# Kernel optimization log

Measured on AMD Instinct MI355X. Metric: run time of the kernel, lower is better.

The kernel has to match this reference:

```python
import jax, jax.numpy as jnp
import numpy as np

INPUT_DIM = 512
MIX = 32
HID = 96
B, T = 256, 512


def setup_inputs() -> dict:
    key = jax.random.key(0)
    ks = jax.random.split(key, 8)
    s = lambda fan_in: 1.0 / np.sqrt(fan_in)
    x = jax.random.normal(ks[0], (B, T, INPUT_DIM), dtype=jnp.float32)
    # mix: Linear(INPUT_DIM, MIX, bias=False) -> weight [MIX, INPUT_DIM]
    W_mix = jax.random.uniform(ks[1], (MIX, INPUT_DIM), jnp.float32, -s(INPUT_DIM), s(INPUT_DIM))
    # GRU layer 0 weights, PyTorch layout: [3H, in], [3H, H], biases [3H]
    W_ih = jax.random.uniform(ks[2], (3 * HID, MIX), jnp.float32, -s(HID), s(HID))
    W_hh = jax.random.uniform(ks[3], (3 * HID, HID), jnp.float32, -s(HID), s(HID))
    b_ih = jax.random.uniform(ks[4], (3 * HID,), jnp.float32, -s(HID), s(HID))
    b_hh = jax.random.uniform(ks[5], (3 * HID,), jnp.float32, -s(HID), s(HID))
    # head: Linear(HID, MIX)
    W_head = jax.random.uniform(ks[6], (MIX, HID), jnp.float32, -s(HID), s(HID))
    b_head = jax.random.uniform(ks[7], (MIX,), jnp.float32, -s(HID), s(HID))
    return {"x": x, "W_mix": W_mix, "W_ih": W_ih, "W_hh": W_hh,
            "b_ih": b_ih, "b_hh": b_hh, "W_head": W_head, "b_head": b_head}


def _gru_last(z, W_ih, W_hh, b_ih, b_hh):
    # z: [B, T, MIX]. Precompute all input-side gate pre-activations: [T, B, 3H]
    gx = jnp.einsum('btm,gm->tbg', z, W_ih) + b_ih
    h0 = jnp.zeros((z.shape[0], HID), dtype=z.dtype)

    def step(h, gx_t):
        gh = h @ W_hh.T + b_hh  # [B, 3H]
        xr, xz, xn = jnp.split(gx_t, 3, axis=-1)
        hr, hz, hn = jnp.split(gh, 3, axis=-1)
        r = jax.nn.sigmoid(xr + hr)
        u = jax.nn.sigmoid(xz + hz)
        n = jnp.tanh(xn + r * hn)
        h_new = (1.0 - u) * n + u * h
        return h_new, None

    h_last, _ = jax.lax.scan(step, h0, gx)
    return h_last  # [B, HID]


def reference(x, W_mix, W_ih, W_hh, b_ih, b_hh, W_head, b_head):
    z = x @ W_mix.T                       # [B, T, MIX]
    last = _gru_last(z, W_ih, W_hh, b_ih, b_hh)  # [B, HID]
    z_next = last @ W_head.T + b_head     # [B, MIX]
    y_next = z_next @ W_mix               # [B, INPUT_DIM] (tied weights)
    return y_next
```

## Files before the change

kernel.cpp:

```cpp
#include <hip/hip_runtime.h>

#define IDIM 512
#define MIXD 32
#define HID 96
#define BB 256
#define TT 512
#define TROWS 32
#define SROW 516

typedef float f32x2 __attribute__((ext_vector_type(2)));
typedef float f32x4 __attribute__((ext_vector_type(4)));

#define EXP2(x) __builtin_amdgcn_exp2f(x)

template <int CTRL>
__device__ __forceinline__ float dpp_shl_add(float x) {
    int m = __builtin_amdgcn_update_dpp(0, __float_as_int(x), CTRL, 0xf, 0xf, true);
    return x + __int_as_float(m);
}
__device__ __forceinline__ float octet_reduce_lane0(float x) {
    x = dpp_shl_add<0x104>(x);
    x = dpp_shl_add<0x102>(x);
    x = dpp_shl_add<0x101>(x);
    return x;
}
__device__ __forceinline__ float red16(float x) {
    x = dpp_shl_add<0x108>(x);
    x = dpp_shl_add<0x104>(x);
    x = dpp_shl_add<0x102>(x);
    x = dpp_shl_add<0x101>(x);
    return x;
}

__global__ __launch_bounds__(256) void k_mix(const float* __restrict__ x,
                                             const float* __restrict__ Wmix,
                                             float* __restrict__ z) {
    __shared__ __align__(16) float sx[TROWS * SROW];
    const int tid = threadIdx.x;
    const int mg = tid >> 4, ks = tid & 15;

    f32x2 w0[16], w1[16];
    #pragma unroll
    for (int i = 0; i < 8; ++i) {
        const int cj = (i + ks) & 7;
        f32x4 v0 = *(const f32x4*)(Wmix + (size_t)(2 * mg)     * IDIM + ks * 32 + cj * 4);
        f32x4 v1 = *(const f32x4*)(Wmix + (size_t)(2 * mg + 1) * IDIM + ks * 32 + cj * 4);
        w0[2*i] = v0.xy; w0[2*i+1] = v0.zw;
        w1[2*i] = v1.xy; w1[2*i+1] = v1.zw;
    }

    const size_t rowbase = (size_t)blockIdx.x * 256;
    const float* xb = x + rowbase * IDIM;

    f32x4 st[16];
    #pragma unroll
    for (int i = 0; i < 16; ++i)
        st[i] = *(const f32x4*)(xb + (size_t)(tid + 256 * i) * 4);

    for (int t = 0; t < 8; ++t) {
        #pragma unroll
        for (int i = 0; i < 16; ++i) {
            const int v = tid + 256 * i, r = v >> 7, c = v & 127;
            *(f32x4*)(&sx[r * SROW + c * 4]) = st[i];
        }
        __syncthreads();

        if (t + 1 < 8) {
            const float* xn = xb + (size_t)(t + 1) * TROWS * IDIM;
            #pragma unroll
            for (int i = 0; i < 16; ++i)
                st[i] = *(const f32x4*)(xn + (size_t)(tid + 256 * i) * 4);
        }

        float* zp = z + (rowbase + (size_t)t * TROWS) * MIXD + 2 * mg;
        for (int r = 0; r < TROWS; ++r) {
            const float* rp = sx + r * SROW + ks * 32;
            f32x2 a0 = {0.f, 0.f}, a1 = {0.f, 0.f};
            #pragma unroll
            for (int i = 0; i < 8; ++i) {
                f32x4 v = *(const f32x4*)(rp + ((i + ks) & 7) * 4);
                a0 = __builtin_elementwise_fma(w0[2*i],   v.xy, a0);
                a0 = __builtin_elementwise_fma(w0[2*i+1], v.zw, a0);
                a1 = __builtin_elementwise_fma(w1[2*i],   v.xy, a1);
                a1 = __builtin_elementwise_fma(w1[2*i+1], v.zw, a1);
            }
            float s0 = red16(a0.x + a0.y);
            float s1 = red16(a1.x + a1.y);
            if (ks == 0) {
                f32x2 o2 = { s0, s1 };
                *(f32x2*)(zp + (size_t)r * MIXD) = o2;
            }
        }
        __syncthreads();
    }
}

__global__ __launch_bounds__(256, 1) void k_scan(const float* __restrict__ z,
                                                 const float* __restrict__ Wih,
                                                 const float* __restrict__ Whh,
                                                 const float* __restrict__ bih,
                                                 const float* __restrict__ bhh,
                                                 const float* __restrict__ Whead,
                                                 const float* __restrict__ bhead,
                                                 const float* __restrict__ Wmix,
                                                 float* __restrict__ y) {
    const int b   = blockIdx.x;
    const int tid = threadIdx.x;
    const int j0  = tid >> 3;
    const int o   = tid & 7;
    const float L  = 1.4426950408889634f;
    const float L2 = 2.8853900817779268f;

    __shared__ __align__(16) float sz[256 * MIXD];
    __shared__ __align__(16) float shp[2][HID];
    __shared__ __align__(16) float szn[MIXD];

    f32x2 whr[3][6], whu[3][6], whn[3][6], wir[3][2], wiu[3][2], win[3][2];
    float br[3], bu[3], bxn[3], bhn[3];
    #pragma unroll
    for (int i = 0; i < 3; ++i) {
        const int j = j0 + 32 * i;
        #pragma unroll
        for (int c = 0; c < 3; ++c) {
            f32x4 v = *(const f32x4*)(Whh + (size_t)(j        ) * HID + o * 12 + c * 4);
            v *= L;  whr[i][2*c] = v.xy; whr[i][2*c+1] = v.zw;
        }
        #pragma unroll
        for (int c = 0; c < 3; ++c) {
            f32x4 v = *(const f32x4*)(Whh + (size_t)(j +   HID) * HID + o * 12 + c * 4);
            v *= L;  whu[i][2*c] = v.xy; whu[i][2*c+1] = v.zw;
        }
        #pragma unroll
        for (int c = 0; c < 3; ++c) {
            f32x4 v = *(const f32x4*)(Whh + (size_t)(j + 2*HID) * HID + o * 12 + c * 4);
            v *= L2; whn[i][2*c] = v.xy; whn[i][2*c+1] = v.zw;
        }
        {
            f32x4 v = *(const f32x4*)(Wih + (size_t)(j        ) * MIXD + o * 4);
            v *= L;  wir[i][0] = v.xy; wir[i][1] = v.zw;
        }
        {
            f32x4 v = *(const f32x4*)(Wih + (size_t)(j +   HID) * MIXD + o * 4);
            v *= L;  wiu[i][0] = v.xy; wiu[i][1] = v.zw;
        }
        {
            f32x4 v = *(const f32x4*)(Wih + (size_t)(j + 2*HID) * MIXD + o * 4);
            v *= L2; win[i][0] = v.xy; win[i][1] = v.zw;
        }
        br[i]  = (o == 0) ? L  * (bih[j]       + bhh[j])       : 0.f;
        bu[i]  = (o == 0) ? L  * (bih[j + HID] + bhh[j + HID]) : 0.f;
        bxn[i] = (o == 0) ? L2 * bih[j + 2*HID] : 0.f;
        bhn[i] = (o == 0) ? L2 * bhh[j + 2*HID] : 0.f;
    }

    float hown[3] = {0.f, 0.f, 0.f};
    if (tid < HID) shp[0][tid] = 0.f;

    const f32x4* zb4 = (const f32x4*)(z + (size_t)b * TT * MIXD);
    f32x4* sz4 = (f32x4*)sz;

    for (int c = 0; c < TT / 256; ++c) {
        #pragma unroll
        for (int i = 0; i < 8; ++i)
            sz4[tid + 256 * i] = zb4[c * 2048 + tid + 256 * i];
        __syncthreads();

        f32x4 z4 = *(const f32x4*)(sz + 0 * MIXD + o * 4);
        for (int tt = 0; tt < 256; ++tt) {
            const int t = (c << 8) + tt;
            const float* hr = shp[t & 1];
            float*       hw = shp[(t + 1) & 1];

            const f32x4 h0 = *(const f32x4*)(hr + o * 12);
            const f32x4 h1 = *(const f32x4*)(hr + o * 12 + 4);
            const f32x4 h2 = *(const f32x4*)(hr + o * 12 + 8);
            const f32x2 hh[6] = { h0.xy, h0.zw, h1.xy, h1.zw, h2.xy, h2.zw };

            float hv[3];
            #pragma unroll
            for (int i = 0; i < 3; ++i) {
                f32x2 aR  = {br[i],  0.f}, aR2  = {0.f, 0.f};
                f32x2 aU  = {bu[i],  0.f}, aU2  = {0.f, 0.f};
                f32x2 aXN = {bxn[i], 0.f};
                f32x2 aHN = {bhn[i], 0.f}, aHN2 = {0.f, 0.f};

                aR  = __builtin_elementwise_fma(wir[i][0], z4.xy, aR);
                aR2 = __builtin_elementwise_fma(wir[i][1], z4.zw, aR2);
                aU  = __builtin_elementwise_fma(wiu[i][0], z4.xy, aU);
                aU2 = __builtin_elementwise_fma(wiu[i][1], z4.zw, aU2);
                aXN = __builtin_elementwise_fma(win[i][0], z4.xy, aXN);
                aXN = __builtin_elementwise_fma(win[i][1], z4.zw, aXN);

                #pragma unroll
                for (int k = 0; k < 3; ++k) {
                    aR   = __builtin_elementwise_fma(whr[i][k],   hh[k],   aR);
                    aR2  = __builtin_elementwise_fma(whr[i][k+3], hh[k+3], aR2);
                    aU   = __builtin_elementwise_fma(whu[i][k],   hh[k],   aU);
                    aU2  = __builtin_elementwise_fma(whu[i][k+3], hh[k+3], aU2);
                    aHN  = __builtin_elementwise_fma(whn[i][k],   hh[k],   aHN);
                    aHN2 = __builtin_elementwise_fma(whn[i][k+3], hh[k+3], aHN2);
                }

                float sR  = octet_reduce_lane0((aR.x  + aR.y)  + (aR2.x  + aR2.y));
                float sU  = octet_reduce_lane0((aU.x  + aU.y)  + (aU2.x  + aU2.y));
                float sXN = octet_reduce_lane0(aXN.x + aXN.y);
                float sHN = octet_reduce_lane0((aHN.x + aHN.y) + (aHN2.x + aHN2.y));

                float r = __builtin_amdgcn_rcpf(1.f + EXP2(-sR));
                float u = __builtin_amdgcn_rcpf(1.f + EXP2(-sU));
                float n = 1.f - 2.f * __builtin_amdgcn_rcpf(1.f + EXP2(sXN + r * sHN));
                hv[i] = u * (hown[i] - n) + n;
                hown[i] = hv[i];
            }
            if (o == 0) {
                hw[j0]      = hv[0];
                hw[j0 + 32] = hv[1];
                hw[j0 + 64] = hv[2];
            }
            f32x4 z4n = z4;
            if (tt + 1 < 256) z4n = *(const f32x4*)(sz + (tt + 1) * MIXD + o * 4);
            __syncthreads();
            z4 = z4n;
        }
    }

    if (tid < MIXD) {
        const float* h = shp[0];
        float a0 = 0.f, a1 = 0.f, a2 = 0.f, a3 = 0.f;
        #pragma unroll
        for (int kc = 0; kc < HID / 4; ++kc) {
            f32x4 wv = *(const f32x4*)(Whead + (size_t)tid * HID + kc * 4);
            f32x4 hv4 = *(const f32x4*)(h + kc * 4);
            a0 += wv.x * hv4.x; a1 += wv.y * hv4.y;
            a2 += wv.z * hv4.z; a3 += wv.w * hv4.w;
        }
        szn[tid] = bhead[tid] + ((a0 + a1) + (a2 + a3));
    }
    __syncthreads();
    #pragma unroll
    for (int rep = 0; rep < 2; ++rep) {
        const int col = tid + 256 * rep;
        float acc = 0.f;
        #pragma unroll
        for (int m = 0; m < MIXD; ++m)
            acc += szn[m] * Wmix[(size_t)m * IDIM + col];
        y[(size_t)b * IDIM + col] = acc;
    }
}

extern "C" void kernel_launch(void* const* d_in, const int* in_sizes, int n_in,
                              void* d_out, int out_size, void* d_ws, size_t ws_size,
                              hipStream_t stream) {
    const float* x     = (const float*)d_in[0];
    const float* Wmix  = (const float*)d_in[1];
    const float* Wih   = (const float*)d_in[2];
    const float* Whh   = (const float*)d_in[3];
    const float* bih   = (const float*)d_in[4];
    const float* bhh   = (const float*)d_in[5];
    const float* Whead = (const float*)d_in[6];
    const float* bhead = (const float*)d_in[7];
    float* out = (float*)d_out;

    float* z = (float*)d_ws;

    k_mix <<<512, 256, 0, stream>>>(x, Wmix, z);
    k_scan<<<BB,  256, 0, stream>>>(z, Wih, Whh, bih, bhh, Whead, bhead, Wmix, out);
}
```

Before: 385.8 us.

## Use inline packed FMA, widen mix outputs per thread, simplify scan accumulators

In the mix kernel, each thread now computes four output columns for half the rows instead of two columns for all rows. This reuses each shared-memory load of x across more FMAs, at the cost of more weight registers. Both kernels now issue v_pk_fma_f32 through inline asm. The scan kernel merges its split accumulators into single chains, which shortens the reductions but lengthens the FMA dependency chains. The scan kernel also loads the z row at the top of each step instead of prefetching it before the barrier, removing the software prefetch.

```diff
diff --git a/kernel.cpp b/kernel.cpp
--- a/kernel.cpp
+++ b/kernel.cpp
@@ -31,22 +31,27 @@
     x = dpp_shl_add<0x101>(x);
     return x;
 }
+__device__ __forceinline__ f32x2 pkfma(f32x2 a, f32x2 b, f32x2 c) {
+    asm("v_pk_fma_f32 %0, %1, %2, %0" : "+v"(c) : "v"(a), "v"(b));
+    return c;
+}
 
 __global__ __launch_bounds__(256) void k_mix(const float* __restrict__ x,
                                              const float* __restrict__ Wmix,
                                              float* __restrict__ z) {
     __shared__ __align__(16) float sx[TROWS * SROW];
     const int tid = threadIdx.x;
-    const int mg = tid >> 4, ks = tid & 15;
-
-    f32x2 w0[16], w1[16];
-    #pragma unroll
-    for (int i = 0; i < 8; ++i) {
-        const int cj = (i + ks) & 7;
-        f32x4 v0 = *(const f32x4*)(Wmix + (size_t)(2 * mg)     * IDIM + ks * 32 + cj * 4);
-        f32x4 v1 = *(const f32x4*)(Wmix + (size_t)(2 * mg + 1) * IDIM + ks * 32 + cj * 4);
-        w0[2*i] = v0.xy; w0[2*i+1] = v0.zw;
-        w1[2*i] = v1.xy; w1[2*i+1] = v1.zw;
+    const int mg = (tid >> 4) & 7, ks = tid & 15, rr = tid >> 7;
+
+    f32x2 w[4][16];
+    #pragma unroll
+    for (int mm = 0; mm < 4; ++mm) {
+        #pragma unroll
+        for (int i = 0; i < 8; ++i) {
+            const int cj = (i + ks) & 7;
+            f32x4 v = *(const f32x4*)(Wmix + (size_t)(4 * mg + mm) * IDIM + ks * 32 + cj * 4);
+            w[mm][2*i] = v.xy; w[mm][2*i+1] = v.zw;
+        }
     }
 
     const size_t rowbase = (size_t)blockIdx.x * 256;
@@ -72,23 +77,26 @@
                 st[i] = *(const f32x4*)(xn + (size_t)(tid + 256 * i) * 4);
         }
 
-        float* zp = z + (rowbase + (size_t)t * TROWS) * MIXD + 2 * mg;
-        for (int r = 0; r < TROWS; ++r) {
+        float* zp = z + (rowbase + (size_t)t * TROWS) * MIXD + 4 * mg;
+        for (int rl = 0; rl < 16; ++rl) {
+            const int r = rr * 16 + rl;
             const float* rp = sx + r * SROW + ks * 32;
-            f32x2 a0 = {0.f, 0.f}, a1 = {0.f, 0.f};
+            f32x2 a0 = {0.f,0.f}, a1 = {0.f,0.f}, a2 = {0.f,0.f}, a3 = {0.f,0.f};
             #pragma unroll
             for (int i = 0; i < 8; ++i) {
                 f32x4 v = *(const f32x4*)(rp + ((i + ks) & 7) * 4);
-                a0 = __builtin_elementwise_fma(w0[2*i],   v.xy, a0);
-                a0 = __builtin_elementwise_fma(w0[2*i+1], v.zw, a0);
-                a1 = __builtin_elementwise_fma(w1[2*i],   v.xy, a1);
-                a1 = __builtin_elementwise_fma(w1[2*i+1], v.zw, a1);
+                a0 = pkfma(w[0][2*i], v.xy, a0); a0 = pkfma(w[0][2*i+1], v.zw, a0);
+                a1 = pkfma(w[1][2*i], v.xy, a1); a1 = pkfma(w[1][2*i+1], v.zw, a1);
+                a2 = pkfma(w[2][2*i], v.xy, a2); a2 = pkfma(w[2][2*i+1], v.zw, a2);
+                a3 = pkfma(w[3][2*i], v.xy, a3); a3 = pkfma(w[3][2*i+1], v.zw, a3);
             }
             float s0 = red16(a0.x + a0.y);
             float s1 = red16(a1.x + a1.y);
+            float s2 = red16(a2.x + a2.y);
+            float s3 = red16(a3.x + a3.y);
             if (ks == 0) {
-                f32x2 o2 = { s0, s1 };
-                *(f32x2*)(zp + (size_t)r * MIXD) = o2;
+                f32x4 o4 = { s0, s1, s2, s3 };
+                *(f32x4*)(zp + (size_t)r * MIXD) = o4;
             }
         }
         __syncthreads();
@@ -165,12 +173,12 @@
             sz4[tid + 256 * i] = zb4[c * 2048 + tid + 256 * i];
         __syncthreads();
 
-        f32x4 z4 = *(const f32x4*)(sz + 0 * MIXD + o * 4);
         for (int tt = 0; tt < 256; ++tt) {
             const int t = (c << 8) + tt;
             const float* hr = shp[t & 1];
             float*       hw = shp[(t + 1) & 1];
 
+            const f32x4 z4 = *(const f32x4*)(sz + tt * MIXD + o * 4);
             const f32x4 h0 = *(const f32x4*)(hr + o * 12);
             const f32x4 h1 = *(const f32x4*)(hr + o * 12 + 4);
             const f32x4 h2 = *(const f32x4*)(hr + o * 12 + 8);
@@ -179,32 +187,27 @@
             float hv[3];
             #pragma unroll
             for (int i = 0; i < 3; ++i) {
-                f32x2 aR  = {br[i],  0.f}, aR2  = {0.f, 0.f};
-                f32x2 aU  = {bu[i],  0.f}, aU2  = {0.f, 0.f};
-                f32x2 aXN = {bxn[i], 0.f};
-                f32x2 aHN = {bhn[i], 0.f}, aHN2 = {0.f, 0.f};
-
-                aR  = __builtin_elementwise_fma(wir[i][0], z4.xy, aR);
-                aR2 = __builtin_elementwise_fma(wir[i][1], z4.zw, aR2);
-                aU  = __builtin_elementwise_fma(wiu[i][0], z4.xy, aU);
-                aU2 = __builtin_elementwise_fma(wiu[i][1], z4.zw, aU2);
-                aXN = __builtin_elementwise_fma(win[i][0], z4.xy, aXN);
-                aXN = __builtin_elementwise_fma(win[i][1], z4.zw, aXN);
+                f32x2 aR  = {br[i],  0.f}, aU  = {bu[i],  0.f};
+                f32x2 aXN = {bxn[i], 0.f}, aHN = {bhn[i], 0.f};
+
+                aR  = pkfma(wir[i][0], z4.xy, aR);
+                aR  = pkfma(wir[i][1], z4.zw, aR);
+                aU  = pkfma(wiu[i][0], z4.xy, aU);
+                aU  = pkfma(wiu[i][1], z4.zw, aU);
+                aXN = pkfma(win[i][0], z4.xy, aXN);
+                aXN = pkfma(win[i][1], z4.zw, aXN);
 
                 #pragma unroll
-                for (int k = 0; k < 3; ++k) {
-                    aR   = __builtin_elementwise_fma(whr[i][k],   hh[k],   aR);
-                    aR2  = __builtin_elementwise_fma(whr[i][k+3], hh[k+3], aR2);
-                    aU   = __builtin_elementwise_fma(whu[i][k],   hh[k],   aU);
-                    aU2  = __builtin_elementwise_fma(whu[i][k+3], hh[k+3], aU2);
-                    aHN  = __builtin_elementwise_fma(whn[i][k],   hh[k],   aHN);
-                    aHN2 = __builtin_elementwise_fma(whn[i][k+3], hh[k+3], aHN2);
+                for (int k = 0; k < 6; ++k) {
+                    aR  = pkfma(whr[i][k], hh[k], aR);
+                    aU  = pkfma(whu[i][k], hh[k], aU);
+                    aHN = pkfma(whn[i][k], hh[k], aHN);
                 }
 
-                float sR  = octet_reduce_lane0((aR.x  + aR.y)  + (aR2.x  + aR2.y));
-                float sU  = octet_reduce_lane0((aU.x  + aU.y)  + (aU2.x  + aU2.y));
+                float sR  = octet_reduce_lane0(aR.x  + aR.y);
+                float sU  = octet_reduce_lane0(aU.x  + aU.y);
                 float sXN = octet_reduce_lane0(aXN.x + aXN.y);
-                float sHN = octet_reduce_lane0((aHN.x + aHN.y) + (aHN2.x + aHN2.y));
+                float sHN = octet_reduce_lane0(aHN.x + aHN.y);
 
                 float r = __builtin_amdgcn_rcpf(1.f + EXP2(-sR));
                 float u = __builtin_amdgcn_rcpf(1.f + EXP2(-sU));
@@ -217,10 +220,7 @@
                 hw[j0 + 32] = hv[1];
                 hw[j0 + 64] = hv[2];
             }
-            f32x4 z4n = z4;
-            if (tt + 1 < 256) z4n = *(const f32x4*)(sz + (tt + 1) * MIXD + o * 4);
             __syncthreads();
-            z4 = z4n;
         }
     }
 
```

Result: faster. 352.8 us (-8.6%).
